# Kernel tuning notes

Measured on AMD Instinct MI355X. Metric: run time of the kernel, lower is better.

## Reference

```python
import jax, jax.numpy as jnp
import numpy as np

MASK_INDEX = 1        # model_config.mask_token_id
TEMPERATURE = 3.0     # config.cat_temperature

B, S, V = 4, 1024, 32000


def setup_inputs() -> dict:
    key = jax.random.key(0)
    k1, k2, k3, k4 = jax.random.split(key, 4)
    logits = jax.random.normal(k1, (B, S, V), dtype=jnp.float32)
    noise = jax.random.uniform(k2, (B, S, V), dtype=jnp.float32, minval=1e-9, maxval=1.0)
    x_t = jax.random.randint(k3, (B, S), 0, 2, dtype=jnp.int32)  # ~half equal MASK_INDEX
    num_transfer_tokens = jax.random.randint(k4, (B,), 0, S, dtype=jnp.int32)
    prompt_length = 128
    return {"logits": logits, "noise": noise, "x_t": x_t,
            "num_transfer_tokens": num_transfer_tokens, "prompt_length": prompt_length}


def reference(logits, noise, x_t, num_transfer_tokens, prompt_length):
    # Gumbel-style noise: exp(logits / T) / (-log(u)), argmax over vocab
    gumbel = -jnp.log(noise)
    noisy = jnp.exp(logits / TEMPERATURE) / gumbel           # [B,S,V]
    x0 = jnp.argmax(noisy, axis=-1)                          # [B,S] int

    # confidence = softmax prob of the sampled token
    p = jax.nn.softmax(logits, axis=-1)                      # [B,S,V]
    conf_p = jnp.take_along_axis(p, x0[..., None], axis=-1)[..., 0]  # [B,S]

    # conf_p[:, prompt_length:] = -inf  (faithful to source)
    col = jnp.arange(S)
    conf_p = jnp.where(col[None, :] >= prompt_length, -jnp.inf, conf_p)

    is_mask = x_t == MASK_INDEX
    x0 = jnp.where(is_mask, x0.astype(x_t.dtype), x_t)
    confidence = jnp.where(is_mask, conf_p, -jnp.inf)

    # per-row variable-k top-k remasking, vectorized via ranks:
    # position is selected iff its descending-confidence rank < k_row
    order = jnp.argsort(-confidence, axis=-1)                # [B,S] indices, desc by conf
    ranks = jnp.argsort(order, axis=-1)                      # rank of each position
    transfer_index = ranks < num_transfer_tokens[:, None]    # [B,S] bool

    x0_new = jnp.where(transfer_index, x0, x_t)              # [B,S]
    return x0_new, confidence
```

## Files before the change

kernel.cpp:

```cpp
#include <hip/hip_runtime.h>
#include <float.h>
#include <math.h>

#define BB 4
#define SS 1024
#define VV 32000
#define MASKTOK 1
#define TEMP 3.0f

#define SCORE_C 0.48089834696298781f

#define CONF_NEG (-1.0e30f)

template<bool NEED_CONF>
__device__ __forceinline__ void scan4(
    float4 l4, float4 u4, int ibase,
    float& best, int& bidx, float& m, float& sum)
{
    float lv[4] = {l4.x, l4.y, l4.z, l4.w};
    float uv[4] = {u4.x, u4.y, u4.z, u4.w};
#pragma unroll
    for (int j = 0; j < 4; ++j) {
        float nl2u = -__log2f(uv[j]);
        float val  = fmaf(lv[j], SCORE_C, -__log2f(nl2u));
        int   idx  = ibase + j;
        if (val > best) { best = val; bidx = idx; }
        if (NEED_CONF) {
            float lvj = lv[j];
            if (lvj > m) { sum *= expf(m - lvj); m = lvj; }
            sum += expf(lvj - m);
        }
    }
}

template<bool NEED_CONF>
__device__ __forceinline__ void row_scan(
    const float4* __restrict__ lg, const float4* __restrict__ nz, int t,
    float& best, int& bidx, float& m, float& sum)
{
#pragma unroll 2
    for (int k = 0; k < 31; ++k) {
        int i = t + k * 256;
        scan4<NEED_CONF>(lg[i], nz[i], i * 4, best, bidx, m, sum);
    }
    if (t < 64) {
        int i = t + 31 * 256;
        scan4<NEED_CONF>(lg[i], nz[i], i * 4, best, bidx, m, sum);
    }
}

__global__ __launch_bounds__(256) void k1_sample(
    const float* __restrict__ logits, const float* __restrict__ noise,
    const int* __restrict__ x_t, const int* __restrict__ pl_ptr,
    int* __restrict__ x0_ws, float* __restrict__ conf_ws)
{
    const int row = blockIdx.x;
    const int t   = threadIdx.x;
    const int s   = row & (SS - 1);

    const int xtv = x_t[row];
    if (xtv != MASKTOK) {
        if (t == 0) { x0_ws[row] = xtv; conf_ws[row] = CONF_NEG; }
        return;
    }
    const bool need_conf = (s < pl_ptr[0]);

    const float4* lg = (const float4*)(logits + (size_t)row * VV);
    const float4* nz = (const float4*)(noise  + (size_t)row * VV);

    float best = -FLT_MAX; int bidx = 0x7fffffff;
    float m = -FLT_MAX, sum = 0.f;

    if (need_conf) row_scan<true >(lg, nz, t, best, bidx, m, sum);
    else           row_scan<false>(lg, nz, t, best, bidx, m, sum);

#pragma unroll
    for (int off = 32; off; off >>= 1) {
        float ob = __shfl_xor(best, off);
        int   oi = __shfl_xor(bidx, off);
        if (ob > best || (ob == best && oi < bidx)) { best = ob; bidx = oi; }
        if (need_conf) {
            float om = __shfl_xor(m,   off);
            float os = __shfl_xor(sum, off);
            float nm = fmaxf(m, om);
            sum = sum * expf(m - nm) + os * expf(om - nm);
            m = nm;
        }
    }

    __shared__ float sb[4]; __shared__ int si[4];
    __shared__ float sm[4]; __shared__ float ssum[4];
    const int wave = t >> 6;
    if ((t & 63) == 0) { sb[wave] = best; si[wave] = bidx; sm[wave] = m; ssum[wave] = sum; }
    __syncthreads();

    if (t == 0) {
        best = sb[0]; bidx = si[0]; m = sm[0]; sum = ssum[0];
#pragma unroll
        for (int w = 1; w < 4; ++w) {
            if (sb[w] > best || (sb[w] == best && si[w] < bidx)) { best = sb[w]; bidx = si[w]; }
            float nm = fmaxf(m, sm[w]);
            sum = sum * expf(m - nm) + ssum[w] * expf(sm[w] - nm);
            m = nm;
        }
        x0_ws[row] = bidx;
        float conf = CONF_NEG;
        if (need_conf) {
            float lx = logits[(size_t)row * VV + bidx];
            conf = expf(lx - m) / sum;
        }
        conf_ws[row] = conf;
    }
}

__global__ __launch_bounds__(256) void k2_select(
    const int* __restrict__ x0_ws, const float* __restrict__ conf_ws,
    const int* __restrict__ x_t, const int* __restrict__ ntt,
    float* __restrict__ out)
{
    const int b   = blockIdx.x;
    const int tid = threadIdx.x;
    const int s   = blockIdx.y * 256 + tid;
    __shared__ float cf[SS];

    ((float4*)cf)[tid] = ((const float4*)(conf_ws + b * SS))[tid];
    __syncthreads();

    const float myconf = cf[s];
    int rank = 0;
    const float4* cf4 = (const float4*)cf;
#pragma unroll 4
    for (int jj = 0; jj < SS / 4; ++jj) {
        float4 c4 = cf4[jj];
        const int jb = jj * 4;
        rank += (c4.x > myconf || (c4.x == myconf && jb + 0 < s)) ? 1 : 0;
        rank += (c4.y > myconf || (c4.y == myconf && jb + 1 < s)) ? 1 : 0;
        rank += (c4.z > myconf || (c4.z == myconf && jb + 2 < s)) ? 1 : 0;
        rank += (c4.w > myconf || (c4.w == myconf && jb + 3 < s)) ? 1 : 0;
    }

    const int  k   = ntt[b];
    const bool sel = rank < k;
    const int  x0  = x0_ws[b * SS + s];
    const int  xtv = x_t[b * SS + s];
    const int  tok = sel ? x0 : xtv;

    float conf_out = fmaxf(myconf, CONF_NEG);

    out[b * SS + s]            = (float)tok;
    out[BB * SS + b * SS + s]  = conf_out;
}

extern "C" void kernel_launch(void* const* d_in, const int* in_sizes, int n_in,
                              void* d_out, int out_size, void* d_ws, size_t ws_size,
                              hipStream_t stream)
{
    const float* logits = (const float*)d_in[0];
    const float* noise  = (const float*)d_in[1];
    const int*   x_t    = (const int*)d_in[2];
    const int*   ntt    = (const int*)d_in[3];
    const int*   pl     = (const int*)d_in[4];
    float* out = (float*)d_out;

    int*   x0_ws   = (int*)d_ws;
    float* conf_ws = (float*)((int*)d_ws + BB * SS);

    k1_sample<<<dim3(BB * SS), dim3(256), 0, stream>>>(logits, noise, x_t, pl, x0_ws, conf_ws);
    k2_select<<<dim3(BB, 4), dim3(256), 0, stream>>>(x0_ws, conf_ws, x_t, ntt, out);
}
```

Baseline: 132.6 us.

## Compact masked rows into a list and process them with a persistent grid

Adds a prepass that atomically builds a list of masked rows and writes default outputs for unmasked rows. The sampling kernel then becomes a grid-strided persistent kernel over the compacted row list, so no blocks are launched only to exit early. The cost is two extra small kernel launches, an atomic counter, and rows whose order in the list is no longer deterministic.

```diff
diff --git a/kernel.cpp b/kernel.cpp
--- a/kernel.cpp
+++ b/kernel.cpp
@@ -7,10 +7,28 @@
 #define VV 32000
 #define MASKTOK 1
 #define TEMP 3.0f
+#define GRID1 2048
 
 #define SCORE_C 0.48089834696298781f
 
 #define CONF_NEG (-1.0e30f)
+
+__global__ void k0_zero(int* __restrict__ nm) { *nm = 0; }
+
+__global__ __launch_bounds__(256) void k0_compact(
+    const int* __restrict__ x_t, int* __restrict__ nm, int* __restrict__ rowlist,
+    int* __restrict__ x0_ws, float* __restrict__ conf_ws)
+{
+    const int r = blockIdx.x * 256 + threadIdx.x;
+    const int xtv = x_t[r];
+    if (xtv == MASKTOK) {
+        int pos = atomicAdd(nm, 1);
+        rowlist[pos] = r;
+    } else {
+        x0_ws[r] = xtv;
+        conf_ws[r] = CONF_NEG;
+    }
+}
 
 template<bool NEED_CONF>
 __device__ __forceinline__ void scan4(
@@ -51,65 +69,67 @@
 
 __global__ __launch_bounds__(256) void k1_sample(
     const float* __restrict__ logits, const float* __restrict__ noise,
-    const int* __restrict__ x_t, const int* __restrict__ pl_ptr,
+    const int* __restrict__ nm_ptr, const int* __restrict__ rowlist,
+    const int* __restrict__ pl_ptr,
     int* __restrict__ x0_ws, float* __restrict__ conf_ws)
 {
-    const int row = blockIdx.x;
-    const int t   = threadIdx.x;
-    const int s   = row & (SS - 1);
-
-    const int xtv = x_t[row];
-    if (xtv != MASKTOK) {
-        if (t == 0) { x0_ws[row] = xtv; conf_ws[row] = CONF_NEG; }
-        return;
-    }
-    const bool need_conf = (s < pl_ptr[0]);
-
-    const float4* lg = (const float4*)(logits + (size_t)row * VV);
-    const float4* nz = (const float4*)(noise  + (size_t)row * VV);
-
-    float best = -FLT_MAX; int bidx = 0x7fffffff;
-    float m = -FLT_MAX, sum = 0.f;
-
-    if (need_conf) row_scan<true >(lg, nz, t, best, bidx, m, sum);
-    else           row_scan<false>(lg, nz, t, best, bidx, m, sum);
-
-#pragma unroll
-    for (int off = 32; off; off >>= 1) {
-        float ob = __shfl_xor(best, off);
-        int   oi = __shfl_xor(bidx, off);
-        if (ob > best || (ob == best && oi < bidx)) { best = ob; bidx = oi; }
-        if (need_conf) {
-            float om = __shfl_xor(m,   off);
-            float os = __shfl_xor(sum, off);
-            float nm = fmaxf(m, om);
-            sum = sum * expf(m - nm) + os * expf(om - nm);
-            m = nm;
-        }
-    }
+    const int t  = threadIdx.x;
+    const int nm = nm_ptr[0];
+    const int pl = pl_ptr[0];
 
     __shared__ float sb[4]; __shared__ int si[4];
     __shared__ float sm[4]; __shared__ float ssum[4];
-    const int wave = t >> 6;
-    if ((t & 63) == 0) { sb[wave] = best; si[wave] = bidx; sm[wave] = m; ssum[wave] = sum; }
-    __syncthreads();
 
-    if (t == 0) {
-        best = sb[0]; bidx = si[0]; m = sm[0]; sum = ssum[0];
+    for (int w = blockIdx.x; w < nm; w += GRID1) {
+        __syncthreads();
+        const int row = rowlist[w];
+        const int s   = row & (SS - 1);
+        const bool need_conf = (s < pl);
+
+        const float4* lg = (const float4*)(logits + (size_t)row * VV);
+        const float4* nz = (const float4*)(noise  + (size_t)row * VV);
+
+        float best = -FLT_MAX; int bidx = 0x7fffffff;
+        float m = -FLT_MAX, sum = 0.f;
+
+        if (need_conf) row_scan<true >(lg, nz, t, best, bidx, m, sum);
+        else           row_scan<false>(lg, nz, t, best, bidx, m, sum);
+
 #pragma unroll
-        for (int w = 1; w < 4; ++w) {
-            if (sb[w] > best || (sb[w] == best && si[w] < bidx)) { best = sb[w]; bidx = si[w]; }
-            float nm = fmaxf(m, sm[w]);
-            sum = sum * expf(m - nm) + ssum[w] * expf(sm[w] - nm);
-            m = nm;
+        for (int off = 32; off; off >>= 1) {
+            float ob = __shfl_xor(best, off);
+            int   oi = __shfl_xor(bidx, off);
+            if (ob > best || (ob == best && oi < bidx)) { best = ob; bidx = oi; }
+            if (need_conf) {
+                float om = __shfl_xor(m,   off);
+                float os = __shfl_xor(sum, off);
+                float nm2 = fmaxf(m, om);
+                sum = sum * expf(m - nm2) + os * expf(om - nm2);
+                m = nm2;
+            }
         }
-        x0_ws[row] = bidx;
-        float conf = CONF_NEG;
-        if (need_conf) {
-            float lx = logits[(size_t)row * VV + bidx];
-            conf = expf(lx - m) / sum;
+
+        const int wave = t >> 6;
+        if ((t & 63) == 0) { sb[wave] = best; si[wave] = bidx; sm[wave] = m; ssum[wave] = sum; }
+        __syncthreads();
+
+        if (t == 0) {
+            best = sb[0]; bidx = si[0]; m = sm[0]; sum = ssum[0];
+#pragma unroll
+            for (int v = 1; v < 4; ++v) {
+                if (sb[v] > best || (sb[v] == best && si[v] < bidx)) { best = sb[v]; bidx = si[v]; }
+                float nm2 = fmaxf(m, sm[v]);
+                sum = sum * expf(m - nm2) + ssum[v] * expf(sm[v] - nm2);
+                m = nm2;
+            }
+            x0_ws[row] = bidx;
+            float conf = CONF_NEG;
+            if (need_conf) {
+                float lx = logits[(size_t)row * VV + bidx];
+                conf = expf(lx - m) / sum;
+            }
+            conf_ws[row] = conf;
         }
-        conf_ws[row] = conf;
     }
 }
 
@@ -162,9 +182,13 @@
     const int*   pl     = (const int*)d_in[4];
     float* out = (float*)d_out;
 
-    int*   x0_ws   = (int*)d_ws;
-    float* conf_ws = (float*)((int*)d_ws + BB * SS);
+    int*   nm      = (int*)d_ws;
+    int*   rowlist = (int*)d_ws + 4;
+    int*   x0_ws   = (int*)d_ws + 4 + BB * SS;
+    float* conf_ws = (float*)((int*)d_ws + 4 + 2 * BB * SS);
 
-    k1_sample<<<dim3(BB * SS), dim3(256), 0, stream>>>(logits, noise, x_t, pl, x0_ws, conf_ws);
+    k0_zero<<<dim3(1), dim3(1), 0, stream>>>(nm);
+    k0_compact<<<dim3(16), dim3(256), 0, stream>>>(x_t, nm, rowlist, x0_ws, conf_ws);
+    k1_sample<<<dim3(GRID1), dim3(256), 0, stream>>>(logits, noise, nm, rowlist, pl, x0_ws, conf_ws);
     k2_select<<<dim3(BB, 4), dim3(256), 0, stream>>>(x0_ws, conf_ws, x_t, ntt, out);
 }
```

New measurement: 134.5 us. No clear change (+1.4%).

## Software-pipeline row scan with double-buffered loads and carry sampled logit

Applied to the files above, without the earlier changes.

Restructures the per-row scan into 16 fully unrolled steps. Each step handles two float4 chunks, and the next step's logits and noise are prefetched into alternating register sets so more loads are in flight. The logit of the winning token is carried through the reductions, which removes the dependent global reload at the end. The kernel also switches to fast __expf and adds a launch-bounds occupancy hint. In exchange, register pressure rises, and the clamped tail chunks are processed twice with their sum contribution suppressed.

```diff
diff --git a/kernel.cpp b/kernel.cpp
--- a/kernel.cpp
+++ b/kernel.cpp
@@ -13,9 +13,9 @@
 #define CONF_NEG (-1.0e30f)
 
 template<bool NEED_CONF>
-__device__ __forceinline__ void scan4(
-    float4 l4, float4 u4, int ibase,
-    float& best, int& bidx, float& m, float& sum)
+__device__ __forceinline__ void do4(
+    float4 l4, float4 u4, int ibase, bool suppress,
+    float& best, int& bidx, float& blog, float& m, float& sum)
 {
     float lv[4] = {l4.x, l4.y, l4.z, l4.w};
     float uv[4] = {u4.x, u4.y, u4.z, u4.w};
@@ -23,12 +23,12 @@
     for (int j = 0; j < 4; ++j) {
         float nl2u = -__log2f(uv[j]);
         float val  = fmaf(lv[j], SCORE_C, -__log2f(nl2u));
-        int   idx  = ibase + j;
-        if (val > best) { best = val; bidx = idx; }
+        if (val > best) { best = val; bidx = ibase + j; blog = lv[j]; }
         if (NEED_CONF) {
             float lvj = lv[j];
-            if (lvj > m) { sum *= expf(m - lvj); m = lvj; }
-            sum += expf(lvj - m);
+            if (lvj > m) { sum *= __expf(m - lvj); m = lvj; }
+            float e = __expf(lvj - m);
+            sum += suppress ? 0.0f : e;
         }
     }
 }
@@ -36,20 +36,33 @@
 template<bool NEED_CONF>
 __device__ __forceinline__ void row_scan(
     const float4* __restrict__ lg, const float4* __restrict__ nz, int t,
-    float& best, int& bidx, float& m, float& sum)
+    float& best, int& bidx, float& blog, float& m, float& sum)
 {
-#pragma unroll 2
-    for (int k = 0; k < 31; ++k) {
-        int i = t + k * 256;
-        scan4<NEED_CONF>(lg[i], nz[i], i * 4, best, bidx, m, sum);
-    }
-    if (t < 64) {
-        int i = t + 31 * 256;
-        scan4<NEED_CONF>(lg[i], nz[i], i * 4, best, bidx, m, sum);
+    float4 la0, la1, ua0, ua1, lb0, lb1, ub0, ub1;
+    la0 = lg[t]; la1 = lg[t + 4096]; ua0 = nz[t]; ua1 = nz[t + 4096];
+
+#pragma unroll
+    for (int k = 0; k < 16; ++k) {
+        if (k + 1 < 16) {
+            int n0 = t + (k + 1) * 256;
+            int n1 = min(n0 + 4096, VV / 4 - 1);
+            if (k & 1) { la0 = lg[n0]; la1 = lg[n1]; ua0 = nz[n0]; ua1 = nz[n1]; }
+            else       { lb0 = lg[n0]; lb1 = lg[n1]; ub0 = nz[n0]; ub1 = nz[n1]; }
+        }
+        int  c0 = t + k * 256;
+        int  c1 = min(c0 + 4096, VV / 4 - 1);
+        bool sup = (c0 + 4096) > (VV / 4 - 1);
+        if (k & 1) {
+            do4<NEED_CONF>(lb0, ub0, c0 * 4, false, best, bidx, blog, m, sum);
+            do4<NEED_CONF>(lb1, ub1, c1 * 4, sup,   best, bidx, blog, m, sum);
+        } else {
+            do4<NEED_CONF>(la0, ua0, c0 * 4, false, best, bidx, blog, m, sum);
+            do4<NEED_CONF>(la1, ua1, c1 * 4, sup,   best, bidx, blog, m, sum);
+        }
     }
 }
 
-__global__ __launch_bounds__(256) void k1_sample(
+__global__ __launch_bounds__(256, 6) void k1_sample(
     const float* __restrict__ logits, const float* __restrict__ noise,
     const int* __restrict__ x_t, const int* __restrict__ pl_ptr,
     int* __restrict__ x0_ws, float* __restrict__ conf_ws)
@@ -68,47 +81,48 @@
     const float4* lg = (const float4*)(logits + (size_t)row * VV);
     const float4* nz = (const float4*)(noise  + (size_t)row * VV);
 
-    float best = -FLT_MAX; int bidx = 0x7fffffff;
+    float best = -FLT_MAX, blog = 0.f; int bidx = 0x7fffffff;
     float m = -FLT_MAX, sum = 0.f;
 
-    if (need_conf) row_scan<true >(lg, nz, t, best, bidx, m, sum);
-    else           row_scan<false>(lg, nz, t, best, bidx, m, sum);
+    if (need_conf) row_scan<true >(lg, nz, t, best, bidx, blog, m, sum);
+    else           row_scan<false>(lg, nz, t, best, bidx, blog, m, sum);
 
 #pragma unroll
     for (int off = 32; off; off >>= 1) {
-        float ob = __shfl_xor(best, off);
-        int   oi = __shfl_xor(bidx, off);
-        if (ob > best || (ob == best && oi < bidx)) { best = ob; bidx = oi; }
+        float ob  = __shfl_xor(best, off);
+        int   oi  = __shfl_xor(bidx, off);
+        float obl = __shfl_xor(blog, off);
+        if (ob > best || (ob == best && oi < bidx)) { best = ob; bidx = oi; blog = obl; }
         if (need_conf) {
             float om = __shfl_xor(m,   off);
             float os = __shfl_xor(sum, off);
             float nm = fmaxf(m, om);
-            sum = sum * expf(m - nm) + os * expf(om - nm);
+            sum = sum * __expf(m - nm) + os * __expf(om - nm);
             m = nm;
         }
     }
 
-    __shared__ float sb[4]; __shared__ int si[4];
+    __shared__ float sb[4]; __shared__ int si[4]; __shared__ float sl[4];
     __shared__ float sm[4]; __shared__ float ssum[4];
     const int wave = t >> 6;
-    if ((t & 63) == 0) { sb[wave] = best; si[wave] = bidx; sm[wave] = m; ssum[wave] = sum; }
+    if ((t & 63) == 0) { sb[wave] = best; si[wave] = bidx; sl[wave] = blog;
+                         sm[wave] = m;   ssum[wave] = sum; }
     __syncthreads();
 
     if (t == 0) {
-        best = sb[0]; bidx = si[0]; m = sm[0]; sum = ssum[0];
+        best = sb[0]; bidx = si[0]; blog = sl[0]; m = sm[0]; sum = ssum[0];
 #pragma unroll
         for (int w = 1; w < 4; ++w) {
-            if (sb[w] > best || (sb[w] == best && si[w] < bidx)) { best = sb[w]; bidx = si[w]; }
+            if (sb[w] > best || (sb[w] == best && si[w] < bidx)) {
+                best = sb[w]; bidx = si[w]; blog = sl[w];
+            }
             float nm = fmaxf(m, sm[w]);
-            sum = sum * expf(m - nm) + ssum[w] * expf(sm[w] - nm);
+            sum = sum * __expf(m - nm) + ssum[w] * __expf(sm[w] - nm);
             m = nm;
         }
         x0_ws[row] = bidx;
         float conf = CONF_NEG;
-        if (need_conf) {
-            float lx = logits[(size_t)row * VV + bidx];
-            conf = expf(lx - m) / sum;
-        }
+        if (need_conf) conf = __expf(blog - m) / sum;
         conf_ws[row] = conf;
     }
 }
```

Measured after the change: 128.3 us. -3.2%, faster.
